# Optimization experiments

Hardware: AMD Instinct MI355X
Metric: run time of the kernel (lower is better)

The kernel has to match this reference:

```python
import jax, jax.numpy as jnp
import numpy as np

GROUPS = 32
EPS = 1e-6

def group_norm(x, gamma, beta):
    # x: [B,C,H,W]
    B, C, H, W = x.shape
    xg = x.reshape(B, GROUPS, C // GROUPS, H, W)
    mu = xg.mean(axis=(2, 3, 4), keepdims=True)
    var = xg.var(axis=(2, 3, 4), keepdims=True)
    xn = ((xg - mu) * jax.lax.rsqrt(var + EPS)).reshape(B, C, H, W)
    return xn * gamma[None, :, None, None] + beta[None, :, None, None]

def setup_inputs() -> dict:
    key = jax.random.key(0)
    ks = jax.random.split(key, 12)
    B, C, H, W = 4, 256, 64, 64
    s = 1.0 / np.sqrt(C)
    return {
        "x": jax.random.normal(ks[0], (B, C, H, W), jnp.float32),
        "gn_gamma": jnp.ones((C,), jnp.float32),
        "gn_beta": jnp.zeros((C,), jnp.float32),
        "wq": jax.random.normal(ks[1], (C, C), jnp.float32) * s,
        "bq": jnp.zeros((C,), jnp.float32),
        "wk": jax.random.normal(ks[2], (C, C), jnp.float32) * s,
        "bk": jnp.zeros((C,), jnp.float32),
        "wv": jax.random.normal(ks[3], (C, C), jnp.float32) * s,
        "bv": jnp.zeros((C,), jnp.float32),
        "wu": jax.random.normal(ks[4], (1, C), jnp.float32) * s,
        "bu": jnp.zeros((1,), jnp.float32),
        "wp": jax.random.normal(ks[5], (C, C), jnp.float32) * s,
        "bp": jnp.zeros((C,), jnp.float32),
    }

def reference(x, gn_gamma, gn_beta, wq, bq, wk, bk, wv, bv, wu, bu, wp, bp):
    B, C, H, W = x.shape
    hw = H * W
    hn = group_norm(x, gn_gamma, gn_beta)          # norm(x); context=x so same norm
    t = hn.reshape(B, C, hw).transpose(0, 2, 1)    # [B, hw, C]
    q = t @ wq.T + bq                              # 1x1 conv == per-token linear
    k = t @ wk.T + bk
    v = t @ wv.T + bv
    u_map = jax.nn.sigmoid(t @ wu.T + bu)          # [B, hw, 1]
    scale = jnp.asarray(C, x.dtype) ** -0.5
    scores = jnp.einsum('bic,bjc->bij', q, k) * scale * u_map.transpose(0, 2, 1)
    attn = jax.nn.softmax(scores, axis=2)          # softmax over keys j
    out = jnp.einsum('bij,bjc->bic', attn, v)      # [B, hw, C]
    out = (out @ wp.T + bp).transpose(0, 2, 1).reshape(B, C, H, W)
    return (x + out, u_map)
```

## Files before the change

kernel.cpp:

```cpp
#include <hip/hip_runtime.h>
#include <cstdint>

#define B_ 4
#define C_ 256
#define HW_ 4096
#define CPG_ 8
#define M_TOT 16384
#define SCALE 0.0625f
#define LOG2E 1.44269504088896f
#define FLASH_LDS 133120

typedef __attribute__((ext_vector_type(4))) float f32x4;
typedef __attribute__((ext_vector_type(16))) float f32x16;
typedef __attribute__((ext_vector_type(8))) unsigned short u16x8;
typedef __attribute__((ext_vector_type(4))) unsigned short u16x4;
typedef __attribute__((ext_vector_type(4))) unsigned int u32x4;
typedef __attribute__((ext_vector_type(8))) __bf16 bf16x8;

static __device__ __forceinline__ unsigned short f2bf(float f) {
  unsigned int u = __builtin_bit_cast(unsigned int, f);
  u += 0x7fffu + ((u >> 16) & 1u);
  return (unsigned short)(u >> 16);
}
static __device__ __forceinline__ float bf2f(unsigned short s) {
  return __builtin_bit_cast(float, ((unsigned int)s) << 16);
}
static __device__ __forceinline__ bf16x8 ldbf8(const unsigned short* p) {
  return __builtin_bit_cast(bf16x8, *(const u16x8*)p);
}
static __device__ __forceinline__ bf16x8 cvt8(const float* p) {
  f32x4 a = *(const f32x4*)p;
  f32x4 b = *(const f32x4*)(p + 4);
  u16x8 r;
  r[0] = f2bf(a[0]); r[1] = f2bf(a[1]); r[2] = f2bf(a[2]); r[3] = f2bf(a[3]);
  r[4] = f2bf(b[0]); r[5] = f2bf(b[1]); r[6] = f2bf(b[2]); r[7] = f2bf(b[3]);
  return __builtin_bit_cast(bf16x8, r);
}
static __device__ __forceinline__ void gload16(const void* g, void* l) {
  __builtin_amdgcn_global_load_lds(
      (const __attribute__((address_space(1))) unsigned int*)g,
      (__attribute__((address_space(3))) unsigned int*)l, 16, 0, 0);
}
static __device__ __forceinline__ unsigned cvtpk(float lo, float hi) {
  unsigned r;
  asm("v_cvt_pk_bf16_f32 %0, %1, %2" : "=v"(r) : "v"(lo), "v"(hi));
  return r;
}

__global__ __launch_bounds__(256) void gn_kernel(const float* __restrict__ x,
    const float* __restrict__ gamma, const float* __restrict__ beta,
    unsigned short* __restrict__ t) {
  int bg = blockIdx.x;
  int b = bg >> 5, g = bg & 31;
  const float* xp = x + ((size_t)(b * C_ + g * CPG_)) * HW_;
  float s = 0.f, ss = 0.f;
  for (int i = threadIdx.x; i < CPG_ * HW_; i += 256) {
    float v = xp[i]; s += v; ss += v * v;
  }
#pragma unroll
  for (int m = 32; m; m >>= 1) { s += __shfl_xor(s, m); ss += __shfl_xor(ss, m); }
  __shared__ float red[8];
  if ((threadIdx.x & 63) == 0) { red[threadIdx.x >> 6] = s; red[4 + (threadIdx.x >> 6)] = ss; }
  __syncthreads();
  float S = red[0] + red[1] + red[2] + red[3];
  float SS = red[4] + red[5] + red[6] + red[7];
  float mean = S * (1.f / 32768.f);
  float var = SS * (1.f / 32768.f) - mean * mean;
  float rs = rsqrtf(var + 1e-6f);
  float gam[CPG_], bet[CPG_];
#pragma unroll
  for (int cc = 0; cc < CPG_; ++cc) {
    float gm = gamma[g * CPG_ + cc];
    gam[cc] = gm * rs;
    bet[cc] = beta[g * CPG_ + cc] - mean * gm * rs;
  }
  for (int sp = threadIdx.x; sp < HW_; sp += 256) {
    u16x8 o;
#pragma unroll
    for (int cc = 0; cc < CPG_; ++cc) {
      float v = xp[cc * HW_ + sp];
      o[cc] = f2bf(v * gam[cc] + bet[cc]);
    }
    *(u16x8*)(t + ((size_t)(b * HW_ + sp)) * C_ + g * CPG_) = o;
  }
}

__global__ __launch_bounds__(256) void u_kernel(const unsigned short* __restrict__ t,
    const float* __restrict__ wu, const float* __restrict__ bu,
    float* __restrict__ uout) {
  int w = threadIdx.x >> 6, l = threadIdx.x & 63;
  int tok = blockIdx.x * 4 + w;
  u16x4 tv = *(const u16x4*)(t + (size_t)tok * C_ + l * 4);
  f32x4 wv4 = *(const f32x4*)(wu + l * 4);
  float d = bf2f(tv[0]) * wv4[0] + bf2f(tv[1]) * wv4[1] +
            bf2f(tv[2]) * wv4[2] + bf2f(tv[3]) * wv4[3];
#pragma unroll
  for (int m = 32; m; m >>= 1) d += __shfl_xor(d, m);
  if (l == 0) uout[tok] = 1.f / (1.f + __expf(-(d + bu[0])));
}

__global__ __launch_bounds__(256, 2) void qkv_kernel(const unsigned short* __restrict__ t,
    const float* __restrict__ wq, const float* __restrict__ wk, const float* __restrict__ wv,
    const float* __restrict__ bq, const float* __restrict__ bk, const float* __restrict__ bv,
    const float* __restrict__ uu,
    unsigned short* __restrict__ q, unsigned short* __restrict__ k,
    unsigned short* __restrict__ vt) {
  int mblk = blockIdx.x, nblk = blockIdx.y;
  int n0 = nblk * 64;
  __shared__ unsigned short WL[64][264];
  __shared__ float lds[64][65];
  int tid = threadIdx.x;
  int wid = tid >> 6, l = tid & 63;
  int lr = l & 15, lg = l >> 4;
  int row = mblk * 64 + wid * 16 + lr;
  bf16x8 af[8];
  const unsigned short* ap = t + (size_t)row * C_ + lg * 8;
#pragma unroll
  for (int kc = 0; kc < 8; ++kc) af[kc] = ldbf8(ap + kc * 32);
  f32x4 u4 = *(const f32x4*)(uu + mblk * 64 + wid * 16 + lg * 4);

#pragma unroll 1
  for (int w = 0; w < 3; ++w) {
    const float* W = w == 0 ? wq : (w == 1 ? wk : wv);
    const float* bias = w == 0 ? bq : (w == 1 ? bk : bv);
    if (w) __syncthreads();
#pragma unroll
    for (int p = 0; p < 8; ++p) {
      int rw = p * 8 + (tid >> 5);
      int kc0 = (tid & 31) * 8;
      *(bf16x8*)&WL[rw][kc0] = cvt8(W + (size_t)(n0 + rw) * C_ + kc0);
    }
    __syncthreads();
    f32x4 acc[4] = {};
#pragma unroll
    for (int kc = 0; kc < 8; ++kc)
#pragma unroll
      for (int j = 0; j < 4; ++j) {
        bf16x8 bb = ldbf8(&WL[j * 16 + lr][kc * 32 + lg * 8]);
        acc[j] = __builtin_amdgcn_mfma_f32_16x16x32_bf16(af[kc], bb, acc[j], 0, 0, 0);
      }
    if (w < 2) {
      unsigned short* dst = w ? k : q;
      float su[4] = {1.f, 1.f, 1.f, 1.f};
      if (w == 1) {
        su[0] = SCALE * LOG2E * u4[0]; su[1] = SCALE * LOG2E * u4[1];
        su[2] = SCALE * LOG2E * u4[2]; su[3] = SCALE * LOG2E * u4[3];
      }
#pragma unroll
      for (int j = 0; j < 4; ++j) {
        int col = n0 + j * 16 + lr;
        float bv_ = bias[col];
#pragma unroll
        for (int r = 0; r < 4; ++r)
          dst[(size_t)(mblk * 64 + wid * 16 + lg * 4 + r) * C_ + col] =
              f2bf((acc[j][r] + bv_) * su[r]);
      }
    } else {
#pragma unroll
      for (int j = 0; j < 4; ++j) {
        float bv_ = bias[n0 + j * 16 + lr];
#pragma unroll
        for (int r = 0; r < 4; ++r)
          lds[wid * 16 + lg * 4 + r][j * 16 + lr] = acc[j][r] + bv_;
      }
      __syncthreads();
      int bb_ = (mblk * 64) >> 12;
      int s0 = (mblk * 64) & 4095;
      int ss = tid & 63, cc0 = tid >> 6;
      for (int cc = cc0; cc < 64; cc += 4)
        vt[((size_t)(bb_ * C_ + n0 + cc)) * HW_ + s0 + ss] = f2bf(lds[ss][cc]);
    }
  }
}

__global__ __launch_bounds__(512, 2) void flash_kernel(const unsigned short* __restrict__ q,
    const unsigned short* __restrict__ k, const unsigned short* __restrict__ vt,
    unsigned short* __restrict__ o) {
  extern __shared__ char smem[];
  float* cmb_m = (float*)(smem + 131072);
  float* cmb_l = (float*)(smem + 131584);
  float* facw  = (float*)(smem + 132096);
  float* scrL  = (float*)(smem + 132608);

  int blk = blockIdx.x;
  int xcd = blk & 7, slot = blk >> 3;
  int b = xcd >> 1;
  int qrow0 = (((xcd & 1) << 5) | slot) * 64;
  int tid = threadIdx.x;
  int wid = tid >> 6, l = tid & 63;
  int l5 = l & 31, hi = l >> 5;

  const unsigned short* kb = k + (size_t)b * HW_ * C_;
  const unsigned short* vb = vt + (size_t)b * C_ * HW_;

  float mrow = -1e30f, lrow = 0.f;
  f32x16 oa[8];

  if (wid >= 4) {
    int role = wid - 4;
    int sh = role & 1;
    bool isK = role < 2;
    int w_ = l >> 2;
    int w0_ = w_ & 1, w1_ = (w_ >> 1) & 1, w2_ = (w_ >> 2) & 1, w3_ = (w_ >> 3) & 1;
    int koffb = (l & 3) * 8;
#define STG(IT, BUFN)                                                           \
    {                                                                           \
      int key0n = sh * 2048 + (IT) * 32;                                        \
      if (isK) {                                                                \
        _Pragma("unroll")                                                       \
        for (int j = 0; j < 16; ++j) {                                          \
          int key = j * 2 + hi;                                                 \
          const unsigned short* g =                                             \
              kb + (size_t)(key0n + key) * C_ + ((l5 * 8) ^ (key * 8));         \
          gload16(g, smem + (BUFN) * 32768 + sh * 16384 + j * 1024);            \
        }                                                                       \
      } else {                                                                  \
        _Pragma("unroll")                                                       \
        for (int j = 0; j < 16; ++j) {                                          \
          int j0 = j & 1;                                                       \
          int ch = (j << 4) | (w3_ << 3) | ((w2_ ^ j0) << 2) |                  \
                   ((w1_ ^ w3_) << 1) | (w0_ ^ w2_ ^ j0);                       \
          int ke = koffb ^ ((ch & 3) << 3);                                     \
          const unsigned short* g = vb + (size_t)ch * HW_ + key0n + ke;         \
          gload16(g, smem + 65536 + (BUFN) * 32768 + sh * 16384 + j * 1024);    \
        }                                                                       \
      }                                                                         \
    }
    STG(0, 0);
    __syncthreads();
    for (int it = 0; it < 64; ++it) {
      if (it + 1 < 64) STG(it + 1, (it + 1) & 1);
      __syncthreads();
    }
#undef STG
  } else {
    int h = wid >> 1, qs = wid & 1;
    bf16x8 qreg[16];
    {
      const unsigned short* qp =
          q + ((size_t)b * HW_ + qrow0 + qs * 32 + l5) * C_ + hi * 8;
#pragma unroll
      for (int cc = 0; cc < 16; ++cc) qreg[cc] = ldbf8(qp + cc * 16);
    }
#pragma unroll
    for (int ct = 0; ct < 8; ++ct)
#pragma unroll
      for (int r = 0; r < 16; ++r) oa[ct][r] = 0.f;
    __syncthreads();

    int kx = l5 << 4;
    int vbase = (l5 * 64) ^ ((l5 >> 2) << 6);
    int ko0 = (hi * 16) ^ ((l & 3) << 4);
    int ko1 = (32 + hi * 16) ^ ((l & 3) << 4);

    for (int it = 0; it < 64; ++it) {
      int buf = it & 1;
      const char* KB = smem + buf * 32768 + h * 16384;
      f32x16 sa, sb;
#pragma unroll
      for (int r = 0; r < 16; ++r) { sa[r] = 0.f; sb[r] = 0.f; }
#pragma unroll
      for (int cc = 0; cc < 16; cc += 2) {
        bf16x8 kf0 = ldbf8((const unsigned short*)(KB + l5 * 512 +
                                                   ((cc * 32 + hi * 16) ^ kx)));
        bf16x8 kf1 = ldbf8((const unsigned short*)(KB + l5 * 512 +
                                                   (((cc + 1) * 32 + hi * 16) ^ kx)));
        sa = __builtin_amdgcn_mfma_f32_32x32x16_bf16(kf0, qreg[cc], sa, 0, 0, 0);
        sb = __builtin_amdgcn_mfma_f32_32x32x16_bf16(kf1, qreg[cc + 1], sb, 0, 0, 0);
      }
      f32x16 s = sa + sb;
      float mxl = s[0];
#pragma unroll
      for (int r = 1; r < 16; ++r) mxl = fmaxf(mxl, s[r]);
      float mx = fmaxf(mxl, __shfl_xor(mxl, 32));
      if (!__all(mx <= mrow + 11.f)) {
        float mnew = fmaxf(mrow, mx);
        float scr = exp2f(mrow - mnew);
        mrow = mnew;
        lrow *= scr;
        if (hi == 0) scrL[wid * 32 + l5] = scr;
        float sr[16];
#pragma unroll
        for (int r = 0; r < 16; ++r)
          sr[r] = scrL[wid * 32 + (r & 3) + 8 * (r >> 2) + 4 * hi];
#pragma unroll
        for (int ct = 0; ct < 8; ++ct)
#pragma unroll
          for (int r = 0; r < 16; ++r) oa[ct][r] *= sr[r];
      }
      unsigned wp[8];
#pragma unroll
      for (int rp = 0; rp < 8; ++rp) {
        float e0 = exp2f(s[2 * rp] - mrow);
        float e1 = exp2f(s[2 * rp + 1] - mrow);
        lrow += e0 + e1;
        wp[rp] = cvtpk(e0, e1);
      }
      unsigned sx[8];
#pragma unroll
      for (int rp = 0; rp < 8; ++rp) sx[rp] = (unsigned)__shfl_xor((int)wp[rp], 32);
      bool hib = (hi != 0);
      u32x4 pa0u = {hib ? sx[2] : wp[0], hib ? sx[3] : wp[1],
                    hib ? wp[2] : sx[0], hib ? wp[3] : sx[1]};
      u32x4 pa1u = {hib ? sx[6] : wp[4], hib ? sx[7] : wp[5],
                    hib ? wp[6] : sx[4], hib ? wp[7] : sx[5]};
      bf16x8 pa0 = __builtin_bit_cast(bf16x8, pa0u);
      bf16x8 pa1 = __builtin_bit_cast(bf16x8, pa1u);
      const char* VB = smem + 65536 + buf * 32768 + h * 16384;
#pragma unroll
      for (int ct = 0; ct < 8; ++ct) {
        bf16x8 v0 = ldbf8((const unsigned short*)(VB + ct * 2048 + vbase + ko0));
        bf16x8 v1 = ldbf8((const unsigned short*)(VB + ct * 2048 + vbase + ko1));
        oa[ct] = __builtin_amdgcn_mfma_f32_32x32x16_bf16(pa0, v0, oa[ct], 0, 0, 0);
        oa[ct] = __builtin_amdgcn_mfma_f32_32x32x16_bf16(pa1, v1, oa[ct], 0, 0, 0);
      }
      __syncthreads();
    }
  }

  float l_all = 0.f;
  if (wid < 4) {
    l_all = lrow + __shfl_xor(lrow, 32);
    if (hi == 0) { cmb_m[wid * 32 + l5] = mrow; cmb_l[wid * 32 + l5] = l_all; }
  }
  __syncthreads();
  if (wid < 4) {
    float mo = cmb_m[(wid ^ 2) * 32 + l5];
    float lo = cmb_l[(wid ^ 2) * 32 + l5];
    float M = fmaxf(mrow, mo);
    float el = exp2f(mrow - M), eo = exp2f(mo - M);
    float fac = el / (l_all * el + lo * eo);
    if (hi == 0) facw[wid * 32 + l5] = fac;
    float fr[16];
#pragma unroll
    for (int r = 0; r < 16; ++r)
      fr[r] = facw[wid * 32 + (r & 3) + 8 * (r >> 2) + 4 * hi];
    float* Ow = (float*)(smem + wid * 32768);
#pragma unroll
    for (int ct = 0; ct < 8; ++ct)
#pragma unroll
      for (int r = 0; r < 16; ++r) {
        int qr = (r & 3) + 8 * (r >> 2) + 4 * hi;
        Ow[qr * 256 + ct * 32 + l5] = oa[ct][r] * fr[r];
      }
  }
  __syncthreads();
  for (int e = tid; e < 2048; e += 512) {
    int row = e >> 5;
    int c8 = (e & 31) * 8;
    int qs_ = row >> 5, q_ = row & 31;
    const float* p0 = (const float*)(smem + qs_ * 32768) + q_ * 256 + c8;
    const float* p1 = (const float*)(smem + (2 + qs_) * 32768) + q_ * 256 + c8;
    u16x8 ov;
#pragma unroll
    for (int j = 0; j < 8; ++j) ov[j] = f2bf(p0[j] + p1[j]);
    *(u16x8*)(o + ((size_t)b * HW_ + qrow0 + row) * C_ + c8) = ov;
  }
}

__global__ __launch_bounds__(256, 2) void proj_kernel(const unsigned short* __restrict__ o,
    const float* __restrict__ wp, const float* __restrict__ bp,
    const float* __restrict__ x, float* __restrict__ y) {
  int mblk = blockIdx.x, nblk = blockIdx.y;
  int n0 = nblk * 64;
  __shared__ unsigned short WL[64][264];
  int tid = threadIdx.x;
#pragma unroll
  for (int p = 0; p < 8; ++p) {
    int row = p * 8 + (tid >> 5);
    int kc0 = (tid & 31) * 8;
    *(bf16x8*)&WL[row][kc0] = cvt8(wp + (size_t)(n0 + row) * C_ + kc0);
  }
  __syncthreads();
  int wid = tid >> 6, l = tid & 63;
  int lr = l & 15, lg = l >> 4;
  int row = mblk * 64 + wid * 16 + lr;
  f32x4 acc[4] = {};
  const unsigned short* ap = o + (size_t)row * C_ + lg * 8;
#pragma unroll
  for (int kc = 0; kc < 8; ++kc) {
    bf16x8 a = ldbf8(ap + kc * 32);
#pragma unroll
    for (int j = 0; j < 4; ++j) {
      bf16x8 bb = ldbf8(&WL[j * 16 + lr][kc * 32 + lg * 8]);
      acc[j] = __builtin_amdgcn_mfma_f32_16x16x32_bf16(a, bb, acc[j], 0, 0, 0);
    }
  }
  __shared__ float lds[64][65];
#pragma unroll
  for (int j = 0; j < 4; ++j) {
    float bv_ = bp[n0 + j * 16 + lr];
#pragma unroll
    for (int r = 0; r < 4; ++r)
      lds[wid * 16 + lg * 4 + r][j * 16 + lr] = acc[j][r] + bv_;
  }
  __syncthreads();
  int bb_ = (mblk * 64) >> 12;
  int s0 = (mblk * 64) & 4095;
  int ss = tid & 63, cc0 = tid >> 6;
  for (int cc = cc0; cc < 64; cc += 4) {
    size_t idx = ((size_t)(bb_ * C_ + n0 + cc)) * HW_ + s0 + ss;
    y[idx] = x[idx] + lds[ss][cc];
  }
}

extern "C" void kernel_launch(void* const* d_in, const int* in_sizes, int n_in,
                              void* d_out, int out_size, void* d_ws, size_t ws_size,
                              hipStream_t stream) {
  const float* x     = (const float*)d_in[0];
  const float* gamma = (const float*)d_in[1];
  const float* beta  = (const float*)d_in[2];
  const float* wq    = (const float*)d_in[3];
  const float* bq    = (const float*)d_in[4];
  const float* wk    = (const float*)d_in[5];
  const float* bk    = (const float*)d_in[6];
  const float* wv    = (const float*)d_in[7];
  const float* bv    = (const float*)d_in[8];
  const float* wu    = (const float*)d_in[9];
  const float* bu    = (const float*)d_in[10];
  const float* wp    = (const float*)d_in[11];
  const float* bp    = (const float*)d_in[12];

  float* y = (float*)d_out;
  float* uout = y + (size_t)B_ * C_ * HW_;

  unsigned short* t  = (unsigned short*)d_ws;
  unsigned short* qb = t + (size_t)M_TOT * C_;
  unsigned short* kk = qb + (size_t)M_TOT * C_;
  unsigned short* vt = kk + (size_t)M_TOT * C_;

  hipFuncSetAttribute((const void*)flash_kernel,
                      hipFuncAttributeMaxDynamicSharedMemorySize, FLASH_LDS);

  gn_kernel<<<128, 256, 0, stream>>>(x, gamma, beta, t);
  u_kernel<<<4096, 256, 0, stream>>>(t, wu, bu, uout);
  qkv_kernel<<<dim3(256, 4), 256, 0, stream>>>(t, wq, wk, wv, bq, bk, bv, uout, qb, kk, vt);
  flash_kernel<<<256, 512, FLASH_LDS, stream>>>(qb, kk, vt, t);
  proj_kernel<<<dim3(256, 4), 256, 0, stream>>>(t, wp, bp, x, y);
}
```

Baseline: 197.1 us.

## Software-pipeline flash loop: defer PV MFMA one iteration, triple-buffer V

The flash kernel now computes QK^T for key tile i while issuing the PV MFMAs for tile i-1. V gets a third LDS buffer (LDS grows to 160KB) so the producer can stay ahead, and s_setprio raises priority around the MFMA block. LDS round trips for broadcasting the rescale and normalization factors are replaced by ds_bpermute, and the two head halves are combined in a single LDS accumulator instead of two buffers. The block-to-batch mapping drops the XCD-aware swizzle. The larger LDS footprint may limit occupancy, and the changed block mapping may hurt L2 locality.

```diff
diff --git a/kernel.cpp b/kernel.cpp
--- a/kernel.cpp
+++ b/kernel.cpp
@@ -8,7 +8,7 @@
 #define M_TOT 16384
 #define SCALE 0.0625f
 #define LOG2E 1.44269504088896f
-#define FLASH_LDS 133120
+#define FLASH_LDS 163840
 
 typedef __attribute__((ext_vector_type(4))) float f32x4;
 typedef __attribute__((ext_vector_type(16))) float f32x16;
@@ -45,6 +45,10 @@
   unsigned r;
   asm("v_cvt_pk_bf16_f32 %0, %1, %2" : "=v"(r) : "v"(lo), "v"(hi));
   return r;
+}
+static __device__ __forceinline__ float bperm(float v, int src) {
+  return __builtin_bit_cast(float,
+      __builtin_amdgcn_ds_bpermute(src << 2, __builtin_bit_cast(int, v)));
 }
 
 __global__ __launch_bounds__(256) void gn_kernel(const float* __restrict__ x,
@@ -179,21 +183,20 @@
   extern __shared__ char smem[];
   float* cmb_m = (float*)(smem + 131072);
   float* cmb_l = (float*)(smem + 131584);
-  float* facw  = (float*)(smem + 132096);
-  float* scrL  = (float*)(smem + 132608);
+  float* Oacc  = (float*)smem;
 
   int blk = blockIdx.x;
-  int xcd = blk & 7, slot = blk >> 3;
-  int b = xcd >> 1;
-  int qrow0 = (((xcd & 1) << 5) | slot) * 64;
+  int b = blk >> 6;
+  int qrow0 = (blk & 63) * 64;
   int tid = threadIdx.x;
   int wid = tid >> 6, l = tid & 63;
   int l5 = l & 31, hi = l >> 5;
+  int h = wid >> 1, qs = wid & 1;
 
   const unsigned short* kb = k + (size_t)b * HW_ * C_;
   const unsigned short* vb = vt + (size_t)b * C_ * HW_;
 
-  float mrow = -1e30f, lrow = 0.f;
+  float mrow = -1e30f, lrow = 0.f, l_all = 0.f;
   f32x16 oa[8];
 
   if (wid >= 4) {
@@ -203,38 +206,43 @@
     int w_ = l >> 2;
     int w0_ = w_ & 1, w1_ = (w_ >> 1) & 1, w2_ = (w_ >> 2) & 1, w3_ = (w_ >> 3) & 1;
     int koffb = (l & 3) * 8;
-#define STG(IT, BUFN)                                                           \
+#define STGK(IT, BUFN)                                                          \
     {                                                                           \
       int key0n = sh * 2048 + (IT) * 32;                                        \
-      if (isK) {                                                                \
-        _Pragma("unroll")                                                       \
-        for (int j = 0; j < 16; ++j) {                                          \
-          int key = j * 2 + hi;                                                 \
-          const unsigned short* g =                                             \
-              kb + (size_t)(key0n + key) * C_ + ((l5 * 8) ^ (key * 8));         \
-          gload16(g, smem + (BUFN) * 32768 + sh * 16384 + j * 1024);            \
-        }                                                                       \
-      } else {                                                                  \
-        _Pragma("unroll")                                                       \
-        for (int j = 0; j < 16; ++j) {                                          \
-          int j0 = j & 1;                                                       \
-          int ch = (j << 4) | (w3_ << 3) | ((w2_ ^ j0) << 2) |                  \
-                   ((w1_ ^ w3_) << 1) | (w0_ ^ w2_ ^ j0);                       \
-          int ke = koffb ^ ((ch & 3) << 3);                                     \
-          const unsigned short* g = vb + (size_t)ch * HW_ + key0n + ke;         \
-          gload16(g, smem + 65536 + (BUFN) * 32768 + sh * 16384 + j * 1024);    \
-        }                                                                       \
+      _Pragma("unroll")                                                         \
+      for (int j = 0; j < 16; ++j) {                                            \
+        int key = j * 2 + hi;                                                   \
+        const unsigned short* g =                                               \
+            kb + (size_t)(key0n + key) * C_ + ((l5 * 8) ^ (key * 8));           \
+        gload16(g, smem + (BUFN) * 32768 + sh * 16384 + j * 1024);              \
       }                                                                         \
     }
-    STG(0, 0);
+#define STGV(IT, BUFN)                                                          \
+    {                                                                           \
+      int key0n = sh * 2048 + (IT) * 32;                                        \
+      _Pragma("unroll")                                                         \
+      for (int j = 0; j < 16; ++j) {                                            \
+        int j0 = j & 1;                                                         \
+        int ch = (j << 4) | (w3_ << 3) | ((w2_ ^ j0) << 2) |                    \
+                 ((w1_ ^ w3_) << 1) | (w0_ ^ w2_ ^ j0);                         \
+        int ke = koffb ^ ((ch & 3) << 3);                                       \
+        const unsigned short* g = vb + (size_t)ch * HW_ + key0n + ke;           \
+        gload16(g, smem + 65536 + (BUFN) * 32768 + sh * 16384 + j * 1024);      \
+      }                                                                         \
+    }
+    if (isK) STGK(0, 0) else STGV(0, 0);
     __syncthreads();
+    int kbn = 1, vbn = 1;
     for (int it = 0; it < 64; ++it) {
-      if (it + 1 < 64) STG(it + 1, (it + 1) & 1);
+      if (it + 1 < 64) {
+        if (isK) { STGK(it + 1, kbn); kbn ^= 1; }
+        else     { STGV(it + 1, vbn); vbn = (vbn == 2) ? 0 : vbn + 1; }
+      }
       __syncthreads();
     }
-#undef STG
+#undef STGK
+#undef STGV
   } else {
-    int h = wid >> 1, qs = wid & 1;
     bf16x8 qreg[16];
     {
       const unsigned short* qp =
@@ -252,41 +260,53 @@
     int vbase = (l5 * 64) ^ ((l5 >> 2) << 6);
     int ko0 = (hi * 16) ^ ((l & 3) << 4);
     int ko1 = (32 + hi * 16) ^ ((l & 3) << 4);
+    bf16x8 paA, paB;
+    int vbp = 0;
 
     for (int it = 0; it < 64; ++it) {
-      int buf = it & 1;
-      const char* KB = smem + buf * 32768 + h * 16384;
-      f32x16 sa, sb;
-#pragma unroll
-      for (int r = 0; r < 16; ++r) { sa[r] = 0.f; sb[r] = 0.f; }
-#pragma unroll
-      for (int cc = 0; cc < 16; cc += 2) {
-        bf16x8 kf0 = ldbf8((const unsigned short*)(KB + l5 * 512 +
-                                                   ((cc * 32 + hi * 16) ^ kx)));
-        bf16x8 kf1 = ldbf8((const unsigned short*)(KB + l5 * 512 +
-                                                   (((cc + 1) * 32 + hi * 16) ^ kx)));
-        sa = __builtin_amdgcn_mfma_f32_32x32x16_bf16(kf0, qreg[cc], sa, 0, 0, 0);
-        sb = __builtin_amdgcn_mfma_f32_32x32x16_bf16(kf1, qreg[cc + 1], sb, 0, 0, 0);
-      }
-      f32x16 s = sa + sb;
-      float mxl = s[0];
-#pragma unroll
-      for (int r = 1; r < 16; ++r) mxl = fmaxf(mxl, s[r]);
+      const char* KB = smem + (it & 1) * 32768 + h * 16384;
+      f32x16 s;
+#pragma unroll
+      for (int r = 0; r < 16; ++r) s[r] = 0.f;
+      __builtin_amdgcn_s_setprio(1);
+#pragma unroll
+      for (int cc = 0; cc < 16; ++cc) {
+        bf16x8 kf = ldbf8((const unsigned short*)(KB + l5 * 512 +
+                                                  ((cc * 32 + hi * 16) ^ kx)));
+        s = __builtin_amdgcn_mfma_f32_32x32x16_bf16(kf, qreg[cc], s, 0, 0, 0);
+      }
+      if (it) {
+        const char* VB = smem + 65536 + vbp * 32768 + h * 16384;
+#pragma unroll
+        for (int ct = 0; ct < 8; ++ct) {
+          bf16x8 v0 = ldbf8((const unsigned short*)(VB + ct * 2048 + vbase + ko0));
+          bf16x8 v1 = ldbf8((const unsigned short*)(VB + ct * 2048 + vbase + ko1));
+          oa[ct] = __builtin_amdgcn_mfma_f32_32x32x16_bf16(paA, v0, oa[ct], 0, 0, 0);
+          oa[ct] = __builtin_amdgcn_mfma_f32_32x32x16_bf16(paB, v1, oa[ct], 0, 0, 0);
+        }
+        vbp = (vbp == 2) ? 0 : vbp + 1;
+      }
+      __builtin_amdgcn_s_setprio(0);
+      float a0 = fmaxf(s[0], s[1]),   a1 = fmaxf(s[2], s[3]);
+      float a2 = fmaxf(s[4], s[5]),   a3 = fmaxf(s[6], s[7]);
+      float a4 = fmaxf(s[8], s[9]),   a5 = fmaxf(s[10], s[11]);
+      float a6 = fmaxf(s[12], s[13]), a7 = fmaxf(s[14], s[15]);
+      float b0 = fmaxf(fmaxf(a0, a1), fmaxf(a2, a3));
+      float b1 = fmaxf(fmaxf(a4, a5), fmaxf(a6, a7));
+      float mxl = fmaxf(b0, b1);
       float mx = fmaxf(mxl, __shfl_xor(mxl, 32));
       if (!__all(mx <= mrow + 11.f)) {
         float mnew = fmaxf(mrow, mx);
         float scr = exp2f(mrow - mnew);
         mrow = mnew;
         lrow *= scr;
-        if (hi == 0) scrL[wid * 32 + l5] = scr;
-        float sr[16];
-#pragma unroll
-        for (int r = 0; r < 16; ++r)
-          sr[r] = scrL[wid * 32 + (r & 3) + 8 * (r >> 2) + 4 * hi];
-#pragma unroll
-        for (int ct = 0; ct < 8; ++ct)
-#pragma unroll
-          for (int r = 0; r < 16; ++r) oa[ct][r] *= sr[r];
+#pragma unroll
+        for (int r = 0; r < 16; ++r) {
+          int qr = (r & 3) + 8 * (r >> 2) + 4 * hi;
+          float sr = bperm(scr, qr);
+#pragma unroll
+          for (int ct = 0; ct < 8; ++ct) oa[ct][r] *= sr;
+        }
       }
       unsigned wp[8];
 #pragma unroll
@@ -304,25 +324,24 @@
                     hib ? wp[2] : sx[0], hib ? wp[3] : sx[1]};
       u32x4 pa1u = {hib ? sx[6] : wp[4], hib ? sx[7] : wp[5],
                     hib ? wp[6] : sx[4], hib ? wp[7] : sx[5]};
-      bf16x8 pa0 = __builtin_bit_cast(bf16x8, pa0u);
-      bf16x8 pa1 = __builtin_bit_cast(bf16x8, pa1u);
-      const char* VB = smem + 65536 + buf * 32768 + h * 16384;
+      paA = __builtin_bit_cast(bf16x8, pa0u);
+      paB = __builtin_bit_cast(bf16x8, pa1u);
+      __syncthreads();
+    }
+    {
+      const char* VB = smem + 65536 + vbp * 32768 + h * 16384;
 #pragma unroll
       for (int ct = 0; ct < 8; ++ct) {
         bf16x8 v0 = ldbf8((const unsigned short*)(VB + ct * 2048 + vbase + ko0));
         bf16x8 v1 = ldbf8((const unsigned short*)(VB + ct * 2048 + vbase + ko1));
-        oa[ct] = __builtin_amdgcn_mfma_f32_32x32x16_bf16(pa0, v0, oa[ct], 0, 0, 0);
-        oa[ct] = __builtin_amdgcn_mfma_f32_32x32x16_bf16(pa1, v1, oa[ct], 0, 0, 0);
-      }
-      __syncthreads();
-    }
-  }
-
-  float l_all = 0.f;
-  if (wid < 4) {
+        oa[ct] = __builtin_amdgcn_mfma_f32_32x32x16_bf16(paA, v0, oa[ct], 0, 0, 0);
+        oa[ct] = __builtin_amdgcn_mfma_f32_32x32x16_bf16(paB, v1, oa[ct], 0, 0, 0);
+      }
+    }
     l_all = lrow + __shfl_xor(lrow, 32);
     if (hi == 0) { cmb_m[wid * 32 + l5] = mrow; cmb_l[wid * 32 + l5] = l_all; }
   }
+
   __syncthreads();
   if (wid < 4) {
     float mo = cmb_m[(wid ^ 2) * 32 + l5];
@@ -330,30 +349,41 @@
     float M = fmaxf(mrow, mo);
     float el = exp2f(mrow - M), eo = exp2f(mo - M);
     float fac = el / (l_all * el + lo * eo);
-    if (hi == 0) facw[wid * 32 + l5] = fac;
-    float fr[16];
-#pragma unroll
-    for (int r = 0; r < 16; ++r)
-      fr[r] = facw[wid * 32 + (r & 3) + 8 * (r >> 2) + 4 * hi];
-    float* Ow = (float*)(smem + wid * 32768);
-#pragma unroll
-    for (int ct = 0; ct < 8; ++ct)
+    if (h == 0) {
 #pragma unroll
       for (int r = 0; r < 16; ++r) {
         int qr = (r & 3) + 8 * (r >> 2) + 4 * hi;
-        Ow[qr * 256 + ct * 32 + l5] = oa[ct][r] * fr[r];
-      }
+        float f_ = bperm(fac, qr);
+#pragma unroll
+        for (int ct = 0; ct < 8; ++ct)
+          Oacc[(qs * 32 + qr) * 256 + ct * 32 + l5] = oa[ct][r] * f_;
+      }
+    }
+  }
+  __syncthreads();
+  if (wid < 4 && h == 1) {
+#pragma unroll
+    for (int r = 0; r < 16; ++r) {
+      int qr = (r & 3) + 8 * (r >> 2) + 4 * hi;
+      float mo = cmb_m[(wid ^ 2) * 32 + l5];
+      float lo = cmb_l[(wid ^ 2) * 32 + l5];
+      float M = fmaxf(mrow, mo);
+      float el = exp2f(mrow - M), eo = exp2f(mo - M);
+      float fac = el / (l_all * el + lo * eo);
+      float f_ = bperm(fac, qr);
+#pragma unroll
+      for (int ct = 0; ct < 8; ++ct)
+        Oacc[(qs * 32 + qr) * 256 + ct * 32 + l5] += oa[ct][r] * f_;
+    }
   }
   __syncthreads();
   for (int e = tid; e < 2048; e += 512) {
     int row = e >> 5;
     int c8 = (e & 31) * 8;
-    int qs_ = row >> 5, q_ = row & 31;
-    const float* p0 = (const float*)(smem + qs_ * 32768) + q_ * 256 + c8;
-    const float* p1 = (const float*)(smem + (2 + qs_) * 32768) + q_ * 256 + c8;
+    const float* p = Oacc + row * 256 + c8;
     u16x8 ov;
 #pragma unroll
-    for (int j = 0; j < 8; ++j) ov[j] = f2bf(p0[j] + p1[j]);
+    for (int j = 0; j < 8; ++j) ov[j] = f2bf(p[j]);
     *(u16x8*)(o + ((size_t)b * HW_ + qrow0 + row) * C_ + c8) = ov;
   }
 }
```

After: 208.0 us. 5.5% more time.
